# Performance work log

Hardware: AMD Instinct MI355X
Metric: run time of the kernel (lower is better)

## Reference

```python
import jax, jax.numpy as jnp
import numpy as np
import math

H_IMG, W_IMG = 800, 1216
STRIDES = [4, 8, 16, 32, 64]
SIZES = [32, 64, 128, 256, 512]
RATIOS = [0.5, 1.0, 2.0]
NUM_PER_LEVEL = [(-(-H_IMG // s)) * (-(-W_IMG // s)) * len(RATIOS) for s in STRIDES]
A_TOTAL = sum(NUM_PER_LEVEL)  # 728973
B = 4
PRE_NMS = 1000   # pre_nms_top_n['testing']
POST_NMS = 1000  # post_nms_top_n['testing']
NMS_TH = 0.7
MIN_SIZE = 1e-3
BBOX_XFORM_CLIP = math.log(1000.0 / 16)
NEG = -1e10
LEVELS_NP = np.repeat(np.arange(len(NUM_PER_LEVEL)), NUM_PER_LEVEL).astype(np.int32)


def _make_anchors():
    out = []
    for stride, size in zip(STRIDES, SIZES):
        fh, fw = -(-H_IMG // stride), -(-W_IMG // stride)
        r = np.sqrt(np.asarray(RATIOS, dtype=np.float64))
        ws, hs = size / r, size * r
        base = np.stack([-ws / 2, -hs / 2, ws / 2, hs / 2], axis=1)  # [3,4]
        sx = np.arange(fw, dtype=np.float64) * stride
        sy = np.arange(fh, dtype=np.float64) * stride
        gy, gx = np.meshgrid(sy, sx, indexing='ij')
        shifts = np.stack([gx.ravel(), gy.ravel(), gx.ravel(), gy.ravel()], axis=1)
        out.append((shifts[:, None, :] + base[None]).reshape(-1, 4))
    return np.concatenate(out, 0).astype(np.float32)


def setup_inputs() -> dict:
    key = jax.random.key(0)
    k1, k2 = jax.random.split(key)
    objectness = jax.random.normal(k1, (B, A_TOTAL), dtype=jnp.float32)
    deltas = jax.random.normal(k2, (B, A_TOTAL, 4), dtype=jnp.float32) * 0.2
    anchors = jnp.asarray(_make_anchors())
    return {'objectness': objectness, 'deltas': deltas, 'anchors': anchors}


def _decode(deltas, anchors):
    # BoxCoder.decode with weights (1,1,1,1)
    wa = anchors[:, 2] - anchors[:, 0]
    ha = anchors[:, 3] - anchors[:, 1]
    cxa = anchors[:, 0] + 0.5 * wa
    cya = anchors[:, 1] + 0.5 * ha
    dx, dy = deltas[..., 0], deltas[..., 1]
    dw = jnp.minimum(deltas[..., 2], BBOX_XFORM_CLIP)
    dh = jnp.minimum(deltas[..., 3], BBOX_XFORM_CLIP)
    cx = dx * wa + cxa
    cy = dy * ha + cya
    w = jnp.exp(dw) * wa
    h = jnp.exp(dh) * ha
    return jnp.stack([cx - 0.5 * w, cy - 0.5 * h, cx + 0.5 * w, cy + 0.5 * h], axis=-1)


def _topk_per_level(obj):
    # _get_top_n_idx: independent top-k within each anchor level, indices offset
    idxs, off = [], 0
    for n in NUM_PER_LEVEL:
        k = min(PRE_NMS, n)
        _, ti = jax.lax.top_k(obj[:, off:off + n], k)
        idxs.append(ti + off)
        off += n
    return jnp.concatenate(idxs, axis=1)


def _pairwise_iou(b):
    area = (b[:, 2] - b[:, 0]) * (b[:, 3] - b[:, 1])
    lt = jnp.maximum(b[:, None, :2], b[None, :, :2])
    rb = jnp.minimum(b[:, None, 2:], b[None, :, 2:])
    wh = jnp.clip(rb - lt, 0.0)
    inter = wh[..., 0] * wh[..., 1]
    return inter / (area[:, None] + area[None, :] - inter)


def _filter_image(boxes, scores, lvl):
    # clip_boxes_to_image
    x1 = jnp.clip(boxes[:, 0], 0.0, W_IMG)
    y1 = jnp.clip(boxes[:, 1], 0.0, H_IMG)
    x2 = jnp.clip(boxes[:, 2], 0.0, W_IMG)
    y2 = jnp.clip(boxes[:, 3], 0.0, H_IMG)
    boxes = jnp.stack([x1, y1, x2, y2], axis=1)
    # remove_small_boxes (as a validity mask; fixed shapes under jit)
    valid = ((x2 - x1) >= MIN_SIZE) & ((y2 - y1) >= MIN_SIZE)
    scores = jnp.where(valid, scores, NEG)
    N = boxes.shape[0]
    # batched_nms: offset boxes per level so levels never overlap
    sg_boxes = jax.lax.stop_gradient(boxes)
    offset = lvl.astype(boxes.dtype) * (sg_boxes.max() + 1.0)
    order = jnp.argsort(-jax.lax.stop_gradient(scores))
    iou = _pairwise_iou(sg_boxes[order] + offset[order][:, None])  # [N,N]
    idx = jnp.arange(N)
    def body(i, keep):
        sup = (iou[i] > NMS_TH) & keep[i] & (idx > i)
        return keep & ~sup
    keep = jax.lax.fori_loop(0, N, body, valid[order])
    # kept entries in score order, then truncate to POST_NMS (fixed shape)
    prio = jnp.where(keep, idx, N)
    sel = jnp.argsort(prio)[:POST_NMS]
    kept = keep[sel]
    src = order[sel]
    out_b = jnp.where(kept[:, None], boxes[src], 0.0)
    out_s = jnp.where(kept, scores[src], NEG)
    return out_b, out_s


def reference(objectness, deltas, anchors):
    proposals = _decode(deltas, anchors)                      # [B,A,4]
    top_idx = _topk_per_level(objectness)                     # [B,5000]
    obj_sel = jnp.take_along_axis(objectness, top_idx, axis=1)
    prop_sel = jnp.take_along_axis(proposals, top_idx[..., None], axis=1)
    lvl_sel = jnp.asarray(LEVELS_NP)[top_idx]
    boxes, scores = jax.vmap(_filter_image)(prop_sel, obj_sel, lvl_sel)
    return boxes, scores  # [B,POST_NMS,4], [B,POST_NMS]
```

## Files before the change

### kernel.cpp

```cpp
#include <hip/hip_runtime.h>
#include <stdint.h>

#pragma clang fp contract(off)

#define B_IMGS   4
#define NLVL     5
#define A_TOTAL  242991
#define NSEL     4741
#define NBUCK    8192
#define BSHIFT   19
#define CAND_CAP 2048
#define POST_NMS 1000
#define NBL      (B_IMGS * NLVL)
#define NMS_TH   0.7f
#define NEGV     (-1e10f)
#define W_IMGF   1216.0f
#define H_IMGF   800.0f
#define MIN_SZ   1e-3f
#define BBOX_CLIP 4.135166556742356f

#define NSLICE_PER_IMG 34

__device__ __forceinline__ int lvl_k(int l) { return (l == 4) ? 741 : 1000; }

__device__ __forceinline__ unsigned flipf(float f) {
    unsigned u = __float_as_uint(f);
    return u ^ (unsigned)(((int)u >> 31) | 0x80000000);
}
__device__ __forceinline__ float unflipf(unsigned os) {
    unsigned u = (os & 0x80000000u) ? (os ^ 0x80000000u) : ~os;
    return __uint_as_float(u);
}

__device__ __forceinline__ void async_cp16(const void* g, void* l) {
    __builtin_amdgcn_global_load_lds(
        (const __attribute__((address_space(1))) unsigned*)g,
        (__attribute__((address_space(3))) unsigned*)l,
        16, 0, 0);
}

static constexpr size_t OFF_BM5   = 0;
static constexpr size_t OFF_CNT   = 128;
static constexpr size_t OFF_HSL   = 256;
static constexpr size_t OFF_PSL   = OFF_HSL  + (size_t)B_IMGS * NSLICE_PER_IMG * NBUCK * 4;
static constexpr size_t OFF_CAND  = OFF_PSL  + (size_t)B_IMGS * NSLICE_PER_IMG * 256 * 4;
static constexpr size_t OFF_SEL   = OFF_CAND + (size_t)NBL * CAND_CAP * 8;
static constexpr size_t OFF_BOXR  = OFF_SEL  + (size_t)B_IMGS * NSEL * 8;
static constexpr size_t OFF_SCR   = OFF_BOXR + (size_t)B_IMGS * NSEL * 16;
static constexpr size_t OFF_BOXL  = OFF_SCR  + (size_t)B_IMGS * NSEL * 4;
static constexpr size_t OFF_VAL   = OFF_BOXL + (size_t)B_IMGS * NSEL * 16;
static constexpr size_t OFF_RMAP  = OFF_VAL  + (size_t)B_IMGS * NSEL * 4;
static constexpr size_t OFF_KEEP  = OFF_RMAP + (size_t)B_IMGS * NSEL * 4;
static constexpr size_t OFF_MASK  = (OFF_KEEP + (size_t)B_IMGS * NSEL * 4 + 15) & ~(size_t)15;
static constexpr size_t WS_NEED   = OFF_MASK + (size_t)NBL * 1024 * 16 * 8;

#define HBLK_PER_IMG 34
__global__ __launch_bounds__(512) void k_hist(const float* __restrict__ obj,
                                              unsigned* __restrict__ hist_sl,
                                              unsigned* __restrict__ part_sl,
                                              unsigned* __restrict__ cnt) {
    __shared__ __align__(16) unsigned lh[NBUCK];
    const int tid = threadIdx.x;
    const int b = blockIdx.x / HBLK_PER_IMG;
    const int r = blockIdx.x - b * HBLK_PER_IMG;
    if (r == 33) {
        if (b == 0 && tid < NBL) cnt[tid] = 0;
        return;
    }
    int sofs, sub, chunk, lstart, n;
    if (r < 24)      { sofs = 0;  sub = r;      chunk = 7600; lstart = 0;      n = 182400; }
    else if (r < 30) { sofs = 24; sub = r - 24; chunk = 7600; lstart = 182400; n = 45600; }
    else if (r < 32) { sofs = 30; sub = r - 30; chunk = 5700; lstart = 228000; n = 11400; }
    else             { sofs = 32; sub = 0;      chunk = 2850; lstart = 239400; n = 2850; }
    #pragma unroll
    for (int i = tid; i < NBUCK; i += 512) lh[i] = 0;
    __syncthreads();
    const int s0 = sub * chunk;
    const int m = min(chunk, n - s0);
    const float* src = obj + (size_t)b * A_TOTAL + lstart + s0;
    const int peel0 = (int)(((16u - ((unsigned)(uintptr_t)src & 15u)) & 15u) >> 2);
    const int peel  = (peel0 < m) ? peel0 : m;
    const int nv    = (m - peel) >> 2;
    const float4* s4 = (const float4*)(src + peel);
    const int tail0 = peel + (nv << 2);
#define H1(f) atomicAdd(&lh[flipf(f) >> BSHIFT], 1u)
#define H4(v) do { H1((v).x); H1((v).y); H1((v).z); H1((v).w); } while (0)
    if (tid < peel) H1(src[tid]);
    for (int i = tid; i < nv; i += 2048) {
        if (i + 1536 < nv) {
            float4 a0 = s4[i], a1 = s4[i + 512], a2 = s4[i + 1024], a3 = s4[i + 1536];
            H4(a0); H4(a1); H4(a2); H4(a3);
        } else {
            float4 a0 = s4[i]; H4(a0);
            if (i + 512  < nv) { float4 a = s4[i + 512];  H4(a); }
            if (i + 1024 < nv) { float4 a = s4[i + 1024]; H4(a); }
        }
    }
    for (int i = tail0 + tid; i < m; i += 512) H1(src[i]);
#undef H4
#undef H1
    __syncthreads();
    const int slice = b * NSLICE_PER_IMG + sofs + sub;
    unsigned* gh = hist_sl + (size_t)slice * NBUCK;
    #pragma unroll
    for (int i = tid; i < NBUCK / 4; i += 512)
        ((uint4*)gh)[i] = ((const uint4*)lh)[i];
    if (tid < 256) {
        unsigned s = 0;
        #pragma unroll
        for (int i = 0; i < 32; ++i) s += lh[tid * 32 + ((i + tid) & 31)];
        part_sl[(size_t)slice * 256 + tid] = s;
    }
}

#define CBLK_PER_IMG 65
__global__ __launch_bounds__(256) void k_compact(const float* __restrict__ obj,
                                                 const unsigned* __restrict__ hist_sl,
                                                 const unsigned* __restrict__ part_sl,
                                                 unsigned* __restrict__ cnt,
                                                 unsigned long long* __restrict__ cand) {
    __shared__ unsigned long long sbuf[CAND_CAP];
    __shared__ unsigned wsum[4];
    __shared__ unsigned fcnt[4];
    __shared__ unsigned s_cum, s_thr, lcnt, gbase;
    const int tid = threadIdx.x;
    const int b = blockIdx.x / CBLK_PER_IMG;
    const int r = blockIdx.x - b * CBLK_PER_IMG;
    int l, sofs, nsub, sub, chunk, lstart, n;
    if (r < 48)      { l = 0; sofs = 0;  nsub = 24; sub = r;      chunk = 3800; lstart = 0;      n = 182400; }
    else if (r < 60) { l = 1; sofs = 24; nsub = 6;  sub = r - 48; chunk = 3800; lstart = 182400; n = 45600; }
    else if (r < 63) { l = 2; sofs = 30; nsub = 2;  sub = r - 60; chunk = 3800; lstart = 228000; n = 11400; }
    else if (r == 63){ l = 3; sofs = 32; nsub = 1;  sub = 0;      chunk = 2850; lstart = 239400; n = 2850; }
    else             { l = 4; sofs = 33; nsub = 0;  sub = 0;      chunk = 741;  lstart = 242250; n = 741; }
    const int bl = b * NLVL + l;
    const int kl = lvl_k(l);
    if (tid == 0) { lcnt = 0; s_cum = 0; }
    __syncthreads();
    unsigned T = 0;
    if (l < 4) {
        const int lane = tid & 63, wv = tid >> 6;
        const unsigned* pb = part_sl + (size_t)(b * NSLICE_PER_IMG + sofs) * 256 + (255 - tid);
        unsigned x = 0;
        #pragma unroll 6
        for (int s = 0; s < nsub; ++s) x += pb[(size_t)s * 256];
        #pragma unroll
        for (int d = 1; d < 64; d <<= 1) {
            unsigned up = __shfl_up(x, d);
            if (lane >= d) x += up;
        }
        if (lane == 63) wsum[wv] = x;
        __syncthreads();
        unsigned add = 0;
        #pragma unroll
        for (int u = 0; u < 3; ++u) if (u < wv) add += wsum[u];
        const unsigned suffix = x + add;
        unsigned long long bm = __ballot(suffix >= (unsigned)kl);
        if (lane == 0) fcnt[wv] = (unsigned)__popcll(bm);
        __syncthreads();
        const int chnk = (int)(fcnt[0] + fcnt[1] + fcnt[2] + fcnt[3]) - 1;
        if ((255 - tid) == chnk + 1) s_cum = suffix;
        __syncthreads();
        if (tid < 64) {
            unsigned y = 0;
            if (tid < 32) {
                const unsigned* hb = hist_sl + (size_t)(b * NSLICE_PER_IMG + sofs) * NBUCK
                                   + chnk * 32 + (31 - tid);
                #pragma unroll 6
                for (int s = 0; s < nsub; ++s) y += hb[(size_t)s * NBUCK];
            }
            #pragma unroll
            for (int d = 1; d < 32; d <<= 1) {
                unsigned up = __shfl_up(y, d);
                if (tid >= d) y += up;
            }
            unsigned suf2 = s_cum + y;
            unsigned long long bm2 = __ballot((tid < 32) && (suf2 >= (unsigned)kl));
            if (tid == 0) {
                int istar = (int)__popcll(bm2) - 1;
                s_thr = (unsigned)(chnk * 32 + istar);
            }
        }
        __syncthreads();
        T = s_thr;
    }
    const int s0 = sub * chunk;
    const int m = min(chunk, n - s0);
    const int abase = lstart + s0;
    const float* src = obj + (size_t)b * A_TOTAL + abase;
    const int peel0 = (int)(((16u - ((unsigned)(uintptr_t)src & 15u)) & 15u) >> 2);
    const int peel  = (peel0 < m) ? peel0 : m;
    const int nv    = (m - peel) >> 2;
    const float4* s4 = (const float4*)(src + peel);
    const int tail0 = peel + (nv << 2);
#define E1(f, idx) do { unsigned os_ = flipf(f); \
    if ((os_ >> BSHIFT) >= T) { \
        unsigned slot = atomicAdd(&lcnt, 1u); \
        if (slot < CAND_CAP) \
            sbuf[slot] = (((unsigned long long)(~os_)) << 32) | (unsigned)(idx); \
    } } while (0)
#define E4(v, gb) do { E1((v).x, (gb)); E1((v).y, (gb) + 1); \
                       E1((v).z, (gb) + 2); E1((v).w, (gb) + 3); } while (0)
    if (tid < peel) E1(src[tid], abase + tid);
    for (int i = tid; i < nv; i += 512) {
        const int gb0 = abase + peel + (i << 2);
        if (i + 256 < nv) {
            float4 a0 = s4[i], a1 = s4[i + 256];
            E4(a0, gb0);
            E4(a1, gb0 + 1024);
        } else {
            float4 a0 = s4[i];
            E4(a0, gb0);
        }
    }
    for (int i = tail0 + tid; i < m; i += 256) E1(src[i], abase + i);
#undef E4
#undef E1
    __syncthreads();
    unsigned total = lcnt; if (total > CAND_CAP) total = CAND_CAP;
    if (tid == 0) gbase = atomicAdd(&cnt[bl], total);
    __syncthreads();
    const unsigned gb = gbase;
    for (unsigned i = tid; i < total; i += 256) {
        unsigned g = gb + i;
        if (g < CAND_CAP)
            cand[(size_t)bl * CAND_CAP + g] = sbuf[i];
    }
}

__global__ __launch_bounds__(1024) void k_sort(const unsigned long long* __restrict__ cand,
                                               const unsigned* __restrict__ cnt,
                                               unsigned long long* __restrict__ sel) {
    __shared__ unsigned long long keys[CAND_CAP];
    const int bl = blockIdx.x;
    const int b = bl / NLVL, l = bl - (bl / NLVL) * NLVL;
    const int tid = threadIdx.x;
    int m = (int)cnt[bl];
    if (m > CAND_CAP) m = CAND_CAP;
    for (int i = tid; i < CAND_CAP; i += 1024)
        keys[i] = (i < m) ? cand[(size_t)bl * CAND_CAP + i] : ~0ULL;
    __syncthreads();
    for (int k = 2; k <= CAND_CAP; k <<= 1) {
        for (int j = k >> 1; j > 0; j >>= 1) {
            int i = ((tid / j) * (j << 1)) + (tid % j);
            int p = i + j;
            bool up = ((i & k) == 0);
            unsigned long long a = keys[i], c = keys[p];
            if ((a > c) == up) { keys[i] = c; keys[p] = a; }
            __syncthreads();
        }
    }
    int kl = lvl_k(l);
    for (int q = tid; q < kl; q += 1024)
        sel[(size_t)b * NSEL + l * 1000 + q] = keys[q];
}

__device__ __forceinline__ int lbound_lds(const unsigned long long* s, int len,
                                          unsigned long long key) {
    int lo = 0, hi = len;
    while (lo < hi) {
        int mid = (lo + hi) >> 1;
        if (s[mid] < key) lo = mid + 1; else hi = mid;
    }
    return lo;
}

__global__ void k_decode(const float* __restrict__ deltas, const float* __restrict__ anchors,
                         const unsigned long long* __restrict__ sel,
                         float* __restrict__ boxes_r, float* __restrict__ score_r,
                         float* __restrict__ boxes_l, int* __restrict__ valid_l,
                         int* __restrict__ rankmap, unsigned* __restrict__ boxmax5) {
    __shared__ unsigned long long skey[NSEL];
    __shared__ float wmax[16];
    const int b = blockIdx.y;
    const int tid = threadIdx.x;
    for (int i = tid; i < NSEL; i += 1024)
        skey[i] = sel[(size_t)b * NSEL + i];
    __syncthreads();

    int p = blockIdx.x * 1024 + tid;
    bool on = p < NSEL;
    float mx = 0.0f;
    if (on) {
        int l = p / 1000;
        int q = p - l * 1000;
        unsigned long long key = skey[p];
        unsigned a = (unsigned)(key & 0xFFFFFFFFu);
        unsigned os = ~((unsigned)(key >> 32));
        if (a >= A_TOTAL) a = 0;
        float score = unflipf(os);
        int r = q;
        for (int l2 = 0; l2 < NLVL; ++l2) {
            if (l2 == l) continue;
            r += lbound_lds(skey + l2 * 1000, lvl_k(l2), key);
        }
        const float* dv = deltas + ((size_t)b * A_TOTAL + a) * 4;
        const float* av = anchors + (size_t)a * 4;
        float ax1 = av[0], ay1 = av[1], ax2 = av[2], ay2 = av[3];
        float wa = ax2 - ax1, ha = ay2 - ay1;
        float cxa = ax1 + 0.5f * wa, cya = ay1 + 0.5f * ha;
        float dx = dv[0], dy = dv[1];
        float dw = fminf(dv[2], BBOX_CLIP), dh = fminf(dv[3], BBOX_CLIP);
        float cx = dx * wa + cxa, cy = dy * ha + cya;
        float w = expf(dw) * wa, h = expf(dh) * ha;
        float x1 = cx - 0.5f * w, y1 = cy - 0.5f * h;
        float x2 = cx + 0.5f * w, y2 = cy + 0.5f * h;
        float x1c = fminf(fmaxf(x1, 0.0f), W_IMGF);
        float y1c = fminf(fmaxf(y1, 0.0f), H_IMGF);
        float x2c = fminf(fmaxf(x2, 0.0f), W_IMGF);
        float y2c = fminf(fmaxf(y2, 0.0f), H_IMGF);
        int valid = ((x2c - x1c) >= MIN_SZ) && ((y2c - y1c) >= MIN_SZ);
        mx = fmaxf(fmaxf(x1c, y1c), fmaxf(x2c, y2c));
        size_t rp = (size_t)b * NSEL + r;
        boxes_r[rp * 4 + 0] = x1c; boxes_r[rp * 4 + 1] = y1c;
        boxes_r[rp * 4 + 2] = x2c; boxes_r[rp * 4 + 3] = y2c;
        score_r[rp] = score;
        size_t pp = (size_t)b * NSEL + p;
        boxes_l[pp * 4 + 0] = x1c; boxes_l[pp * 4 + 1] = y1c;
        boxes_l[pp * 4 + 2] = x2c; boxes_l[pp * 4 + 3] = y2c;
        valid_l[pp] = valid;
        rankmap[pp] = r;
    }
    #pragma unroll
    for (int o = 32; o > 0; o >>= 1)
        mx = fmaxf(mx, __shfl_xor(mx, o));
    if ((tid & 63) == 0) wmax[tid >> 6] = mx;
    __syncthreads();
    if (tid == 0) {
        float m2 = wmax[0];
        #pragma unroll
        for (int i = 1; i < 16; ++i) m2 = fmaxf(m2, wmax[i]);
        boxmax5[b * 5 + blockIdx.x] = __float_as_uint(m2);
    }
}

__global__ void k_mask(const float* __restrict__ boxes_l, const unsigned* __restrict__ boxmax5,
                       unsigned long long* __restrict__ mask) {
    int bl = blockIdx.z;
    int b = bl / NLVL, l = bl - b * NLVL;
    int kl = lvl_k(l);
    int w = blockIdx.x, rg = blockIdx.y, tid = threadIdx.x;
    if (rg * 256 >= kl) return;
    float M = __uint_as_float(boxmax5[b * 5 + 0]);
    #pragma unroll
    for (int j = 1; j < 5; ++j) M = fmaxf(M, __uint_as_float(boxmax5[b * 5 + j]));
    M += 1.0f;
    float off = (float)l * M;
    __shared__ float cb[64][5];
    int j0 = w * 64;
    if (tid < 64) {
        int j = j0 + tid;
        if (j < kl) {
            const float* bp = boxes_l + ((size_t)b * NSEL + l * 1000 + j) * 4;
            float x1 = bp[0] + off, y1 = bp[1] + off, x2 = bp[2] + off, y2 = bp[3] + off;
            cb[tid][0] = x1; cb[tid][1] = y1; cb[tid][2] = x2; cb[tid][3] = y2;
            cb[tid][4] = (x2 - x1) * (y2 - y1);
        }
    }
    __syncthreads();
    int i = rg * 256 + tid;
    if (i >= kl) return;
    unsigned long long word = 0;
    if (j0 + 63 > i) {
        const float* bp = boxes_l + ((size_t)b * NSEL + l * 1000 + i) * 4;
        float ix1 = bp[0] + off, iy1 = bp[1] + off, ix2 = bp[2] + off, iy2 = bp[3] + off;
        float ai = (ix2 - ix1) * (iy2 - iy1);
        int jmax = min(64, kl - j0);
        for (int bb = 0; bb < jmax; ++bb) {
            int jj = j0 + bb;
            if (jj <= i) continue;
            float ltx = fmaxf(ix1, cb[bb][0]), lty = fmaxf(iy1, cb[bb][1]);
            float rbx = fminf(ix2, cb[bb][2]), rby = fminf(iy2, cb[bb][3]);
            float ww = fmaxf(rbx - ltx, 0.0f), hh = fmaxf(rby - lty, 0.0f);
            float inter = ww * hh;
            float iou = inter / ((ai + cb[bb][4]) - inter);
            if (iou > NMS_TH) word |= (1ULL << bb);
        }
    }
    mask[((size_t)bl * 1024 + i) * 16 + w] = word;
}

__global__ void k_resolve(const int* __restrict__ valid_l, const int* __restrict__ rankmap,
                          const unsigned long long* __restrict__ mask, int* __restrict__ keep_r) {
    const int bl = blockIdx.x;
    const int b = bl / NLVL, l = bl - b * NLVL;
    const int kl = lvl_k(l);
    const int lane = threadIdx.x;
    __shared__ __align__(16) unsigned long long sbufA[64 * 16];
    __shared__ __align__(16) unsigned long long sbufB[64 * 16];
    const int base = b * NSEL + l * 1000;

    unsigned long long keep_w = 0;
    for (int c = 0; c < 16; ++c) {
        int q = c * 64 + lane;
        int vv = (q < kl) ? valid_l[base + q] : 0;
        unsigned long long bm = __ballot(vv);
        if (lane == c) keep_w = bm;
    }

    const int nch = (kl + 63) >> 6;
    const char* mbyte = (const char*)(mask + (size_t)bl * 1024 * 16);

    {
        const char* g0 = mbyte + (size_t)lane * 16;
        #pragma unroll
        for (int j = 0; j < 8; ++j)
            async_cp16(g0 + j * 1024, (char*)sbufA + j * 1024);
    }

    for (int c = 0; c < nch; ++c) {
        unsigned long long* cur = (c & 1) ? sbufB : sbufA;
        unsigned long long* nxt = (c & 1) ? sbufA : sbufB;
        __syncthreads();
        if (c + 1 < nch) {
            const char* g1 = mbyte + (size_t)(c + 1) * 8192 + (size_t)lane * 16;
            #pragma unroll
            for (int j = 0; j < 8; ++j)
                async_cp16(g1 + j * 1024, (char*)nxt + j * 1024);
        }
        unsigned long long kw = __shfl(keep_w, c);
        if (kw) {
            unsigned long long diag = cur[lane * 16 + c];
            unsigned dlo = (unsigned)diag, dhi = (unsigned)(diag >> 32);
            unsigned long long nz = __ballot(diag != 0ULL);
            unsigned long long rem = kw & nz;
            while (rem) {
                int r = __ffsll((long long)rem) - 1;
                unsigned lo = __builtin_amdgcn_readlane(dlo, r);
                unsigned hi = __builtin_amdgcn_readlane(dhi, r);
                unsigned long long d = ((unsigned long long)hi << 32) | lo;
                kw &= ~d;
                rem &= ~(d | (1ULL << r));
            }
            unsigned long long supp = 0;
            if (lane < 16) {
                #pragma unroll
                for (int r = 0; r < 64; ++r) {
                    unsigned long long m = cur[r * 16 + lane];
                    supp |= (((kw >> r) & 1ULL) ? m : 0ULL);
                }
            }
            if (lane == c) keep_w = kw;
            else if (lane < 16 && lane > c) keep_w &= ~supp;
        }
    }
    __syncthreads();
    for (int c = 0; c < 16; ++c) {
        unsigned long long kwc = __shfl(keep_w, c);
        int q = c * 64 + lane;
        if (q < kl)
            keep_r[b * NSEL + rankmap[base + q]] = (int)((kwc >> lane) & 1ULL);
    }
}

__global__ void k_output(const int* __restrict__ keep_r, const float* __restrict__ boxes_r,
                         const float* __restrict__ score_r, float* __restrict__ out) {
    int b = blockIdx.x, tid = threadIdx.x;
    float* ob = out + (size_t)b * POST_NMS * 4;
    float* osc = out + (size_t)B_IMGS * POST_NMS * 4 + (size_t)b * POST_NMS;
    for (int p = tid; p < POST_NMS; p += 1024) {
        ob[p * 4 + 0] = 0.0f; ob[p * 4 + 1] = 0.0f;
        ob[p * 4 + 2] = 0.0f; ob[p * 4 + 3] = 0.0f;
        osc[p] = NEGV;
    }
    __syncthreads();
    const int CH = 5;
    int base = tid * CH;
    int cnt = 0;
    #pragma unroll
    for (int k = 0; k < CH; ++k) {
        int r = base + k;
        if (r < NSEL) cnt += keep_r[b * NSEL + r];
    }
    __shared__ int ps[1024];
    ps[tid] = cnt;
    __syncthreads();
    for (int ofs = 1; ofs < 1024; ofs <<= 1) {
        int v = (tid >= ofs) ? ps[tid - ofs] : 0;
        __syncthreads();
        ps[tid] += v;
        __syncthreads();
    }
    int p = ps[tid] - cnt;
    #pragma unroll
    for (int k = 0; k < CH; ++k) {
        int r = base + k;
        if (r < NSEL && keep_r[b * NSEL + r]) {
            if (p < POST_NMS) {
                const float* bp = boxes_r + ((size_t)b * NSEL + r) * 4;
                ob[p * 4 + 0] = bp[0]; ob[p * 4 + 1] = bp[1];
                ob[p * 4 + 2] = bp[2]; ob[p * 4 + 3] = bp[3];
                osc[p] = score_r[(size_t)b * NSEL + r];
            }
            ++p;
        }
    }
}

extern "C" void kernel_launch(void* const* d_in, const int* in_sizes, int n_in,
                              void* d_out, int out_size, void* d_ws, size_t ws_size,
                              hipStream_t stream) {
    const float* obj     = (const float*)d_in[0];
    const float* deltas  = (const float*)d_in[1];
    const float* anchors = (const float*)d_in[2];
    float* out = (float*)d_out;

    char* ws = (char*)d_ws;
    unsigned*            boxmax5 = (unsigned*)(ws + OFF_BM5);
    unsigned*            cnt     = (unsigned*)(ws + OFF_CNT);
    unsigned*            hist_sl = (unsigned*)(ws + OFF_HSL);
    unsigned*            part_sl = (unsigned*)(ws + OFF_PSL);
    unsigned long long*  cand    = (unsigned long long*)(ws + OFF_CAND);
    unsigned long long*  sel     = (unsigned long long*)(ws + OFF_SEL);
    float*               boxes_r = (float*)(ws + OFF_BOXR);
    float*               score_r = (float*)(ws + OFF_SCR);
    float*               boxes_l = (float*)(ws + OFF_BOXL);
    int*                 valid_l = (int*)(ws + OFF_VAL);
    int*                 rankmap = (int*)(ws + OFF_RMAP);
    int*                 keep_r  = (int*)(ws + OFF_KEEP);
    unsigned long long*  maskp   = (unsigned long long*)(ws + OFF_MASK);

    (void)in_sizes; (void)n_in; (void)out_size; (void)ws_size; (void)WS_NEED;

    k_hist<<<B_IMGS * HBLK_PER_IMG, 512, 0, stream>>>(obj, hist_sl, part_sl, cnt);
    k_compact<<<B_IMGS * CBLK_PER_IMG, 256, 0, stream>>>(obj, hist_sl, part_sl, cnt, cand);
    k_sort<<<NBL, 1024, 0, stream>>>(cand, cnt, sel);
    k_decode<<<dim3(5, B_IMGS), 1024, 0, stream>>>(
        deltas, anchors, sel, boxes_r, score_r, boxes_l, valid_l, rankmap, boxmax5);
    k_mask<<<dim3(16, 4, NBL), 256, 0, stream>>>(boxes_l, boxmax5, maskp);
    k_resolve<<<NBL, 64, 0, stream>>>(valid_l, rankmap, maskp, keep_r);
    k_output<<<B_IMGS, 1024, 0, stream>>>(keep_r, boxes_r, score_r, out);
}
```

Baseline: 176.4 us.

## Fuse mask, resolve and output kernels via last-block-done atomic counters

Merges the IoU mask kernel, the per-level NMS resolve kernel and the output compaction kernel into one launch. Each mask block bumps a per-(image,level) counter, and the last block to arrive runs the greedy resolve. A second per-image counter then lets the last level block write the compacted output. This removes two kernel launches and their gaps. In exchange the resolve and output phases now run inside a 256-thread block that is mostly idle, and correctness relies on threadfence and atomic ordering plus counter zeroing in k_hist.

```diff
diff --git a/kernel.cpp b/kernel.cpp
--- a/kernel.cpp
+++ b/kernel.cpp
@@ -41,7 +41,9 @@
 
 static constexpr size_t OFF_BM5   = 0;
 static constexpr size_t OFF_CNT   = 128;
-static constexpr size_t OFF_HSL   = 256;
+static constexpr size_t OFF_DONE1 = 208;
+static constexpr size_t OFF_DONE2 = 288;
+static constexpr size_t OFF_HSL   = 320;
 static constexpr size_t OFF_PSL   = OFF_HSL  + (size_t)B_IMGS * NSLICE_PER_IMG * NBUCK * 4;
 static constexpr size_t OFF_CAND  = OFF_PSL  + (size_t)B_IMGS * NSLICE_PER_IMG * 256 * 4;
 static constexpr size_t OFF_SEL   = OFF_CAND + (size_t)NBL * CAND_CAP * 8;
@@ -58,13 +60,13 @@
 __global__ __launch_bounds__(512) void k_hist(const float* __restrict__ obj,
                                               unsigned* __restrict__ hist_sl,
                                               unsigned* __restrict__ part_sl,
-                                              unsigned* __restrict__ cnt) {
+                                              unsigned* __restrict__ cntz) {
     __shared__ __align__(16) unsigned lh[NBUCK];
     const int tid = threadIdx.x;
     const int b = blockIdx.x / HBLK_PER_IMG;
     const int r = blockIdx.x - b * HBLK_PER_IMG;
     if (r == 33) {
-        if (b == 0 && tid < NBL) cnt[tid] = 0;
+        if (b == 0 && tid < NBL + NBL + B_IMGS) cntz[tid] = 0;
         return;
     }
     int sofs, sub, chunk, lstart, n;
@@ -333,163 +335,190 @@
     }
 }
 
-__global__ void k_mask(const float* __restrict__ boxes_l, const unsigned* __restrict__ boxmax5,
-                       unsigned long long* __restrict__ mask) {
-    int bl = blockIdx.z;
-    int b = bl / NLVL, l = bl - b * NLVL;
-    int kl = lvl_k(l);
-    int w = blockIdx.x, rg = blockIdx.y, tid = threadIdx.x;
-    if (rg * 256 >= kl) return;
-    float M = __uint_as_float(boxmax5[b * 5 + 0]);
-    #pragma unroll
-    for (int j = 1; j < 5; ++j) M = fmaxf(M, __uint_as_float(boxmax5[b * 5 + j]));
-    M += 1.0f;
-    float off = (float)l * M;
+__global__ __launch_bounds__(256) void k_maskro(const float* __restrict__ boxes_l,
+                                                const unsigned* __restrict__ boxmax5,
+                                                unsigned long long* __restrict__ mask,
+                                                const int* __restrict__ valid_l,
+                                                const int* __restrict__ rankmap,
+                                                int* __restrict__ keep_r,
+                                                unsigned* __restrict__ done1,
+                                                unsigned* __restrict__ done2,
+                                                const float* __restrict__ boxes_r,
+                                                const float* __restrict__ score_r,
+                                                float* __restrict__ out) {
     __shared__ float cb[64][5];
-    int j0 = w * 64;
-    if (tid < 64) {
-        int j = j0 + tid;
-        if (j < kl) {
-            const float* bp = boxes_l + ((size_t)b * NSEL + l * 1000 + j) * 4;
-            float x1 = bp[0] + off, y1 = bp[1] + off, x2 = bp[2] + off, y2 = bp[3] + off;
-            cb[tid][0] = x1; cb[tid][1] = y1; cb[tid][2] = x2; cb[tid][3] = y2;
-            cb[tid][4] = (x2 - x1) * (y2 - y1);
-        }
-    }
-    __syncthreads();
-    int i = rg * 256 + tid;
-    if (i >= kl) return;
-    unsigned long long word = 0;
-    if (j0 + 63 > i) {
-        const float* bp = boxes_l + ((size_t)b * NSEL + l * 1000 + i) * 4;
-        float ix1 = bp[0] + off, iy1 = bp[1] + off, ix2 = bp[2] + off, iy2 = bp[3] + off;
-        float ai = (ix2 - ix1) * (iy2 - iy1);
-        int jmax = min(64, kl - j0);
-        for (int bb = 0; bb < jmax; ++bb) {
-            int jj = j0 + bb;
-            if (jj <= i) continue;
-            float ltx = fmaxf(ix1, cb[bb][0]), lty = fmaxf(iy1, cb[bb][1]);
-            float rbx = fminf(ix2, cb[bb][2]), rby = fminf(iy2, cb[bb][3]);
-            float ww = fmaxf(rbx - ltx, 0.0f), hh = fmaxf(rby - lty, 0.0f);
-            float inter = ww * hh;
-            float iou = inter / ((ai + cb[bb][4]) - inter);
-            if (iou > NMS_TH) word |= (1ULL << bb);
-        }
-    }
-    mask[((size_t)bl * 1024 + i) * 16 + w] = word;
-}
-
-__global__ void k_resolve(const int* __restrict__ valid_l, const int* __restrict__ rankmap,
-                          const unsigned long long* __restrict__ mask, int* __restrict__ keep_r) {
-    const int bl = blockIdx.x;
+    __shared__ __align__(16) unsigned long long sbufA[64 * 16];
+    __shared__ __align__(16) unsigned long long sbufB[64 * 16];
+    __shared__ int ps[256];
+    __shared__ int s_flag;
+    const int bl = blockIdx.z;
     const int b = bl / NLVL, l = bl - b * NLVL;
     const int kl = lvl_k(l);
-    const int lane = threadIdx.x;
-    __shared__ __align__(16) unsigned long long sbufA[64 * 16];
-    __shared__ __align__(16) unsigned long long sbufB[64 * 16];
+    const int w = blockIdx.x, rg = blockIdx.y;
+    const int tid = threadIdx.x;
+    const bool act = (rg * 256 < kl);
+
+    if (act) {
+        float M = __uint_as_float(boxmax5[b * 5 + 0]);
+        #pragma unroll
+        for (int j = 1; j < 5; ++j) M = fmaxf(M, __uint_as_float(boxmax5[b * 5 + j]));
+        M += 1.0f;
+        float off = (float)l * M;
+        int j0 = w * 64;
+        if (tid < 64) {
+            int j = j0 + tid;
+            if (j < kl) {
+                const float* bp = boxes_l + ((size_t)b * NSEL + l * 1000 + j) * 4;
+                float x1 = bp[0] + off, y1 = bp[1] + off, x2 = bp[2] + off, y2 = bp[3] + off;
+                cb[tid][0] = x1; cb[tid][1] = y1; cb[tid][2] = x2; cb[tid][3] = y2;
+                cb[tid][4] = (x2 - x1) * (y2 - y1);
+            }
+        }
+        __syncthreads();
+        int i = rg * 256 + tid;
+        if (i < kl) {
+            unsigned long long word = 0;
+            if (j0 + 63 > i) {
+                const float* bp = boxes_l + ((size_t)b * NSEL + l * 1000 + i) * 4;
+                float ix1 = bp[0] + off, iy1 = bp[1] + off, ix2 = bp[2] + off, iy2 = bp[3] + off;
+                float ai = (ix2 - ix1) * (iy2 - iy1);
+                int jmax = min(64, kl - j0);
+                for (int bb = 0; bb < jmax; ++bb) {
+                    int jj = j0 + bb;
+                    if (jj <= i) continue;
+                    float ltx = fmaxf(ix1, cb[bb][0]), lty = fmaxf(iy1, cb[bb][1]);
+                    float rbx = fminf(ix2, cb[bb][2]), rby = fminf(iy2, cb[bb][3]);
+                    float ww = fmaxf(rbx - ltx, 0.0f), hh = fmaxf(rby - lty, 0.0f);
+                    float inter = ww * hh;
+                    float iou = inter / ((ai + cb[bb][4]) - inter);
+                    if (iou > NMS_TH) word |= (1ULL << bb);
+                }
+            }
+            mask[((size_t)bl * 1024 + i) * 16 + w] = word;
+        }
+    }
+
+    __syncthreads();
+    if (tid == 0) {
+        __threadfence();
+        unsigned old = __hip_atomic_fetch_add(done1 + bl, 1u,
+                                              __ATOMIC_ACQ_REL, __HIP_MEMORY_SCOPE_AGENT);
+        s_flag = (old == 63);
+        if (old == 63) __threadfence();
+    }
+    __syncthreads();
+    if (!s_flag) return;
+
+    const int lane = tid & 63;
     const int base = b * NSEL + l * 1000;
-
-    unsigned long long keep_w = 0;
-    for (int c = 0; c < 16; ++c) {
-        int q = c * 64 + lane;
-        int vv = (q < kl) ? valid_l[base + q] : 0;
-        unsigned long long bm = __ballot(vv);
-        if (lane == c) keep_w = bm;
-    }
-
     const int nch = (kl + 63) >> 6;
     const char* mbyte = (const char*)(mask + (size_t)bl * 1024 * 16);
-
-    {
+    unsigned long long keep_w = 0;
+    if (tid < 64) {
+        for (int c = 0; c < 16; ++c) {
+            int q = c * 64 + lane;
+            int vv = (q < kl) ? valid_l[base + q] : 0;
+            unsigned long long bm = __ballot(vv);
+            if (lane == c) keep_w = bm;
+        }
         const char* g0 = mbyte + (size_t)lane * 16;
         #pragma unroll
         for (int j = 0; j < 8; ++j)
             async_cp16(g0 + j * 1024, (char*)sbufA + j * 1024);
     }
-
     for (int c = 0; c < nch; ++c) {
-        unsigned long long* cur = (c & 1) ? sbufB : sbufA;
-        unsigned long long* nxt = (c & 1) ? sbufA : sbufB;
-        __syncthreads();
-        if (c + 1 < nch) {
-            const char* g1 = mbyte + (size_t)(c + 1) * 8192 + (size_t)lane * 16;
-            #pragma unroll
-            for (int j = 0; j < 8; ++j)
-                async_cp16(g1 + j * 1024, (char*)nxt + j * 1024);
-        }
-        unsigned long long kw = __shfl(keep_w, c);
-        if (kw) {
-            unsigned long long diag = cur[lane * 16 + c];
-            unsigned dlo = (unsigned)diag, dhi = (unsigned)(diag >> 32);
-            unsigned long long nz = __ballot(diag != 0ULL);
-            unsigned long long rem = kw & nz;
-            while (rem) {
-                int r = __ffsll((long long)rem) - 1;
-                unsigned lo = __builtin_amdgcn_readlane(dlo, r);
-                unsigned hi = __builtin_amdgcn_readlane(dhi, r);
-                unsigned long long d = ((unsigned long long)hi << 32) | lo;
-                kw &= ~d;
-                rem &= ~(d | (1ULL << r));
-            }
-            unsigned long long supp = 0;
-            if (lane < 16) {
+        __syncthreads();
+        if (tid < 64) {
+            unsigned long long* cur = (c & 1) ? sbufB : sbufA;
+            unsigned long long* nxt = (c & 1) ? sbufA : sbufB;
+            if (c + 1 < nch) {
+                const char* g1 = mbyte + (size_t)(c + 1) * 8192 + (size_t)lane * 16;
                 #pragma unroll
-                for (int r = 0; r < 64; ++r) {
-                    unsigned long long m = cur[r * 16 + lane];
-                    supp |= (((kw >> r) & 1ULL) ? m : 0ULL);
+                for (int j = 0; j < 8; ++j)
+                    async_cp16(g1 + j * 1024, (char*)nxt + j * 1024);
+            }
+            unsigned long long kw = __shfl(keep_w, c);
+            if (kw) {
+                unsigned long long diag = cur[lane * 16 + c];
+                unsigned dlo = (unsigned)diag, dhi = (unsigned)(diag >> 32);
+                unsigned long long nz = __ballot(diag != 0ULL);
+                unsigned long long rem = kw & nz;
+                while (rem) {
+                    int rr = __ffsll((long long)rem) - 1;
+                    unsigned lo = __builtin_amdgcn_readlane(dlo, rr);
+                    unsigned hi = __builtin_amdgcn_readlane(dhi, rr);
+                    unsigned long long d = ((unsigned long long)hi << 32) | lo;
+                    kw &= ~d;
+                    rem &= ~(d | (1ULL << rr));
                 }
-            }
-            if (lane == c) keep_w = kw;
-            else if (lane < 16 && lane > c) keep_w &= ~supp;
-        }
-    }
-    __syncthreads();
-    for (int c = 0; c < 16; ++c) {
-        unsigned long long kwc = __shfl(keep_w, c);
-        int q = c * 64 + lane;
-        if (q < kl)
-            keep_r[b * NSEL + rankmap[base + q]] = (int)((kwc >> lane) & 1ULL);
-    }
-}
-
-__global__ void k_output(const int* __restrict__ keep_r, const float* __restrict__ boxes_r,
-                         const float* __restrict__ score_r, float* __restrict__ out) {
-    int b = blockIdx.x, tid = threadIdx.x;
+                unsigned long long supp = 0;
+                if (lane < 16) {
+                    #pragma unroll
+                    for (int rr = 0; rr < 64; ++rr) {
+                        unsigned long long mm = cur[rr * 16 + lane];
+                        supp |= (((kw >> rr) & 1ULL) ? mm : 0ULL);
+                    }
+                }
+                if (lane == c) keep_w = kw;
+                else if (lane < 16 && lane > c) keep_w &= ~supp;
+            }
+        }
+    }
+    __syncthreads();
+    if (tid < 64) {
+        for (int c = 0; c < 16; ++c) {
+            unsigned long long kwc = __shfl(keep_w, c);
+            int q = c * 64 + lane;
+            if (q < kl)
+                keep_r[b * NSEL + rankmap[base + q]] = (int)((kwc >> lane) & 1ULL);
+        }
+    }
+    __syncthreads();
+
+    if (tid == 0) {
+        __threadfence();
+        unsigned old = __hip_atomic_fetch_add(done2 + b, 1u,
+                                              __ATOMIC_ACQ_REL, __HIP_MEMORY_SCOPE_AGENT);
+        s_flag = (old == NLVL - 1);
+        if (old == NLVL - 1) __threadfence();
+    }
+    __syncthreads();
+    if (!s_flag) return;
+
     float* ob = out + (size_t)b * POST_NMS * 4;
     float* osc = out + (size_t)B_IMGS * POST_NMS * 4 + (size_t)b * POST_NMS;
-    for (int p = tid; p < POST_NMS; p += 1024) {
+    for (int p = tid; p < POST_NMS; p += 256) {
         ob[p * 4 + 0] = 0.0f; ob[p * 4 + 1] = 0.0f;
         ob[p * 4 + 2] = 0.0f; ob[p * 4 + 3] = 0.0f;
         osc[p] = NEGV;
     }
     __syncthreads();
-    const int CH = 5;
-    int base = tid * CH;
-    int cnt = 0;
+    const int CH = 19;
+    int basei = tid * CH;
+    int c0 = 0;
     #pragma unroll
     for (int k = 0; k < CH; ++k) {
-        int r = base + k;
-        if (r < NSEL) cnt += keep_r[b * NSEL + r];
-    }
-    __shared__ int ps[1024];
-    ps[tid] = cnt;
-    __syncthreads();
-    for (int ofs = 1; ofs < 1024; ofs <<= 1) {
+        int rr = basei + k;
+        if (rr < NSEL) c0 += keep_r[b * NSEL + rr];
+    }
+    ps[tid] = c0;
+    __syncthreads();
+    for (int ofs = 1; ofs < 256; ofs <<= 1) {
         int v = (tid >= ofs) ? ps[tid - ofs] : 0;
         __syncthreads();
         ps[tid] += v;
         __syncthreads();
     }
-    int p = ps[tid] - cnt;
+    int p = ps[tid] - c0;
     #pragma unroll
     for (int k = 0; k < CH; ++k) {
-        int r = base + k;
-        if (r < NSEL && keep_r[b * NSEL + r]) {
+        int rr = basei + k;
+        if (rr < NSEL && keep_r[b * NSEL + rr]) {
             if (p < POST_NMS) {
-                const float* bp = boxes_r + ((size_t)b * NSEL + r) * 4;
+                const float* bp = boxes_r + ((size_t)b * NSEL + rr) * 4;
                 ob[p * 4 + 0] = bp[0]; ob[p * 4 + 1] = bp[1];
                 ob[p * 4 + 2] = bp[2]; ob[p * 4 + 3] = bp[3];
-                osc[p] = score_r[(size_t)b * NSEL + r];
+                osc[p] = score_r[(size_t)b * NSEL + rr];
             }
             ++p;
         }
@@ -507,6 +536,8 @@
     char* ws = (char*)d_ws;
     unsigned*            boxmax5 = (unsigned*)(ws + OFF_BM5);
     unsigned*            cnt     = (unsigned*)(ws + OFF_CNT);
+    unsigned*            done1   = (unsigned*)(ws + OFF_DONE1);
+    unsigned*            done2   = (unsigned*)(ws + OFF_DONE2);
     unsigned*            hist_sl = (unsigned*)(ws + OFF_HSL);
     unsigned*            part_sl = (unsigned*)(ws + OFF_PSL);
     unsigned long long*  cand    = (unsigned long long*)(ws + OFF_CAND);
@@ -526,7 +557,7 @@
     k_sort<<<NBL, 1024, 0, stream>>>(cand, cnt, sel);
     k_decode<<<dim3(5, B_IMGS), 1024, 0, stream>>>(
         deltas, anchors, sel, boxes_r, score_r, boxes_l, valid_l, rankmap, boxmax5);
-    k_mask<<<dim3(16, 4, NBL), 256, 0, stream>>>(boxes_l, boxmax5, maskp);
-    k_resolve<<<NBL, 64, 0, stream>>>(valid_l, rankmap, maskp, keep_r);
-    k_output<<<B_IMGS, 1024, 0, stream>>>(keep_r, boxes_r, score_r, out);
-}
+    k_maskro<<<dim3(16, 4, NBL), 256, 0, stream>>>(
+        boxes_l, boxmax5, maskp, valid_l, rankmap, keep_r, done1, done2,
+        boxes_r, score_r, out);
+}
```

New measurement: 240.9 us. +36.5%, slower.

## Fuse per-level sort and decode with per-image grid barrier; stage resolve inputs in LDS

Applied to the files above, without the earlier changes.

Merges the bitonic sort kernel and the decode kernel into one launch of 20 blocks. The five level blocks of each image synchronise through a global atomic counter, which k_hist zeroes along with cnt. This removes one kernel launch and the gap between the two stages. The resolve kernel also preloads valid flags and rank maps into shared memory, overlapping that with the first async mask copy. The spin barrier assumes all 20 blocks are co-resident, which holds given their number, and it adds atomic polling.

```diff
diff --git a/kernel.cpp b/kernel.cpp
--- a/kernel.cpp
+++ b/kernel.cpp
@@ -41,6 +41,8 @@
 
 static constexpr size_t OFF_BM5   = 0;
 static constexpr size_t OFF_CNT   = 128;
+static constexpr size_t OFF_DI    = 208;
+static constexpr size_t OFF_D2    = 224;
 static constexpr size_t OFF_HSL   = 256;
 static constexpr size_t OFF_PSL   = OFF_HSL  + (size_t)B_IMGS * NSLICE_PER_IMG * NBUCK * 4;
 static constexpr size_t OFF_CAND  = OFF_PSL  + (size_t)B_IMGS * NSLICE_PER_IMG * 256 * 4;
@@ -58,13 +60,13 @@
 __global__ __launch_bounds__(512) void k_hist(const float* __restrict__ obj,
                                               unsigned* __restrict__ hist_sl,
                                               unsigned* __restrict__ part_sl,
-                                              unsigned* __restrict__ cnt) {
+                                              unsigned* __restrict__ cntz) {
     __shared__ __align__(16) unsigned lh[NBUCK];
     const int tid = threadIdx.x;
     const int b = blockIdx.x / HBLK_PER_IMG;
     const int r = blockIdx.x - b * HBLK_PER_IMG;
     if (r == 33) {
-        if (b == 0 && tid < NBL) cnt[tid] = 0;
+        if (b == 0 && tid < 28) cntz[tid] = 0;
         return;
     }
     int sofs, sub, chunk, lstart, n;
@@ -227,33 +229,6 @@
     }
 }
 
-__global__ __launch_bounds__(1024) void k_sort(const unsigned long long* __restrict__ cand,
-                                               const unsigned* __restrict__ cnt,
-                                               unsigned long long* __restrict__ sel) {
-    __shared__ unsigned long long keys[CAND_CAP];
-    const int bl = blockIdx.x;
-    const int b = bl / NLVL, l = bl - (bl / NLVL) * NLVL;
-    const int tid = threadIdx.x;
-    int m = (int)cnt[bl];
-    if (m > CAND_CAP) m = CAND_CAP;
-    for (int i = tid; i < CAND_CAP; i += 1024)
-        keys[i] = (i < m) ? cand[(size_t)bl * CAND_CAP + i] : ~0ULL;
-    __syncthreads();
-    for (int k = 2; k <= CAND_CAP; k <<= 1) {
-        for (int j = k >> 1; j > 0; j >>= 1) {
-            int i = ((tid / j) * (j << 1)) + (tid % j);
-            int p = i + j;
-            bool up = ((i & k) == 0);
-            unsigned long long a = keys[i], c = keys[p];
-            if ((a > c) == up) { keys[i] = c; keys[p] = a; }
-            __syncthreads();
-        }
-    }
-    int kl = lvl_k(l);
-    for (int q = tid; q < kl; q += 1024)
-        sel[(size_t)b * NSEL + l * 1000 + q] = keys[q];
-}
-
 __device__ __forceinline__ int lbound_lds(const unsigned long long* s, int len,
                                           unsigned long long key) {
     int lo = 0, hi = len;
@@ -264,25 +239,64 @@
     return lo;
 }
 
-__global__ void k_decode(const float* __restrict__ deltas, const float* __restrict__ anchors,
-                         const unsigned long long* __restrict__ sel,
-                         float* __restrict__ boxes_r, float* __restrict__ score_r,
-                         float* __restrict__ boxes_l, int* __restrict__ valid_l,
-                         int* __restrict__ rankmap, unsigned* __restrict__ boxmax5) {
-    __shared__ unsigned long long skey[NSEL];
+__global__ __launch_bounds__(1024) void k_sortdec(
+        const unsigned long long* __restrict__ cand, const unsigned* __restrict__ cnt,
+        unsigned long long* __restrict__ sel,
+        const float* __restrict__ deltas, const float* __restrict__ anchors,
+        float* __restrict__ boxes_r, float* __restrict__ score_r,
+        float* __restrict__ boxes_l, int* __restrict__ valid_l,
+        int* __restrict__ rankmap, unsigned* __restrict__ boxmax5,
+        unsigned* __restrict__ bar_i) {
+    __shared__ __align__(16) char smem[38016];
     __shared__ float wmax[16];
-    const int b = blockIdx.y;
+    const int bl = blockIdx.x;
+    const int b = bl / NLVL, l = bl - (bl / NLVL) * NLVL;
     const int tid = threadIdx.x;
+
+    {
+        unsigned long long* keys = (unsigned long long*)smem;
+        int m = (int)cnt[bl];
+        if (m > CAND_CAP) m = CAND_CAP;
+        for (int i = tid; i < CAND_CAP; i += 1024)
+            keys[i] = (i < m) ? cand[(size_t)bl * CAND_CAP + i] : ~0ULL;
+        __syncthreads();
+        for (int k = 2; k <= CAND_CAP; k <<= 1) {
+            for (int j = k >> 1; j > 0; j >>= 1) {
+                int i = ((tid / j) * (j << 1)) + (tid % j);
+                int p = i + j;
+                bool up = ((i & k) == 0);
+                unsigned long long a = keys[i], c = keys[p];
+                if ((a > c) == up) { keys[i] = c; keys[p] = a; }
+                __syncthreads();
+            }
+        }
+        int kl = lvl_k(l);
+        for (int q = tid; q < kl; q += 1024)
+            sel[(size_t)b * NSEL + l * 1000 + q] = keys[q];
+    }
+    __syncthreads();
+
+    if (tid == 0) {
+        __threadfence();
+        __hip_atomic_fetch_add(bar_i + b, 1u, __ATOMIC_RELAXED, __HIP_MEMORY_SCOPE_AGENT);
+        while (__hip_atomic_load(bar_i + b, __ATOMIC_RELAXED, __HIP_MEMORY_SCOPE_AGENT)
+               < (unsigned)NLVL)
+            __builtin_amdgcn_s_sleep(2);
+        __threadfence();
+    }
+    __syncthreads();
+
+    unsigned long long* skey = (unsigned long long*)smem;
     for (int i = tid; i < NSEL; i += 1024)
         skey[i] = sel[(size_t)b * NSEL + i];
     __syncthreads();
-
-    int p = blockIdx.x * 1024 + tid;
+    const int sub = l;
+    int p = sub * 1024 + tid;
     bool on = p < NSEL;
     float mx = 0.0f;
     if (on) {
-        int l = p / 1000;
-        int q = p - l * 1000;
+        int l2i = p / 1000;
+        int q = p - l2i * 1000;
         unsigned long long key = skey[p];
         unsigned a = (unsigned)(key & 0xFFFFFFFFu);
         unsigned os = ~((unsigned)(key >> 32));
@@ -290,7 +304,7 @@
         float score = unflipf(os);
         int r = q;
         for (int l2 = 0; l2 < NLVL; ++l2) {
-            if (l2 == l) continue;
+            if (l2 == l2i) continue;
             r += lbound_lds(skey + l2 * 1000, lvl_k(l2), key);
         }
         const float* dv = deltas + ((size_t)b * A_TOTAL + a) * 4;
@@ -329,7 +343,7 @@
         float m2 = wmax[0];
         #pragma unroll
         for (int i = 1; i < 16; ++i) m2 = fmaxf(m2, wmax[i]);
-        boxmax5[b * 5 + blockIdx.x] = __float_as_uint(m2);
+        boxmax5[b * 5 + sub] = __float_as_uint(m2);
     }
 }
 
@@ -387,14 +401,13 @@
     const int lane = threadIdx.x;
     __shared__ __align__(16) unsigned long long sbufA[64 * 16];
     __shared__ __align__(16) unsigned long long sbufB[64 * 16];
+    __shared__ int sval[1000];
+    __shared__ int srnk[1000];
     const int base = b * NSEL + l * 1000;
 
-    unsigned long long keep_w = 0;
-    for (int c = 0; c < 16; ++c) {
-        int q = c * 64 + lane;
-        int vv = (q < kl) ? valid_l[base + q] : 0;
-        unsigned long long bm = __ballot(vv);
-        if (lane == c) keep_w = bm;
+    for (int i = lane; i < 1000; i += 64) {
+        sval[i] = valid_l[base + i];
+        srnk[i] = rankmap[base + i];
     }
 
     const int nch = (kl + 63) >> 6;
@@ -406,11 +419,20 @@
         for (int j = 0; j < 8; ++j)
             async_cp16(g0 + j * 1024, (char*)sbufA + j * 1024);
     }
+    __syncthreads();
+
+    unsigned long long keep_w = 0;
+    for (int c = 0; c < 16; ++c) {
+        int q = c * 64 + lane;
+        int vv = (q < kl) ? sval[q] : 0;
+        unsigned long long bm = __ballot(vv);
+        if (lane == c) keep_w = bm;
+    }
 
     for (int c = 0; c < nch; ++c) {
         unsigned long long* cur = (c & 1) ? sbufB : sbufA;
         unsigned long long* nxt = (c & 1) ? sbufA : sbufB;
-        __syncthreads();
+        if (c > 0) __syncthreads();
         if (c + 1 < nch) {
             const char* g1 = mbyte + (size_t)(c + 1) * 8192 + (size_t)lane * 16;
             #pragma unroll
@@ -448,7 +470,7 @@
         unsigned long long kwc = __shfl(keep_w, c);
         int q = c * 64 + lane;
         if (q < kl)
-            keep_r[b * NSEL + rankmap[base + q]] = (int)((kwc >> lane) & 1ULL);
+            keep_r[b * NSEL + srnk[q]] = (int)((kwc >> lane) & 1ULL);
     }
 }
 
@@ -507,6 +529,7 @@
     char* ws = (char*)d_ws;
     unsigned*            boxmax5 = (unsigned*)(ws + OFF_BM5);
     unsigned*            cnt     = (unsigned*)(ws + OFF_CNT);
+    unsigned*            bar_i   = (unsigned*)(ws + OFF_DI);
     unsigned*            hist_sl = (unsigned*)(ws + OFF_HSL);
     unsigned*            part_sl = (unsigned*)(ws + OFF_PSL);
     unsigned long long*  cand    = (unsigned long long*)(ws + OFF_CAND);
@@ -523,9 +546,9 @@
 
     k_hist<<<B_IMGS * HBLK_PER_IMG, 512, 0, stream>>>(obj, hist_sl, part_sl, cnt);
     k_compact<<<B_IMGS * CBLK_PER_IMG, 256, 0, stream>>>(obj, hist_sl, part_sl, cnt, cand);
-    k_sort<<<NBL, 1024, 0, stream>>>(cand, cnt, sel);
-    k_decode<<<dim3(5, B_IMGS), 1024, 0, stream>>>(
-        deltas, anchors, sel, boxes_r, score_r, boxes_l, valid_l, rankmap, boxmax5);
+    k_sortdec<<<NBL, 1024, 0, stream>>>(cand, cnt, sel, deltas, anchors,
+                                        boxes_r, score_r, boxes_l, valid_l,
+                                        rankmap, boxmax5, bar_i);
     k_mask<<<dim3(16, 4, NBL), 256, 0, stream>>>(boxes_l, boxmax5, maskp);
     k_resolve<<<NBL, 64, 0, stream>>>(valid_l, rankmap, maskp, keep_r);
     k_output<<<B_IMGS, 1024, 0, stream>>>(keep_r, boxes_r, score_r, out);
```

New measurement: 176.9 us. Within noise of the previous version (+0.3%).
